# Kernel tuning notes

Hardware: AMD Instinct MI355X
Metric: run time of the kernel (lower is better)

The kernel has to match this reference:

```python
import jax, jax.numpy as jnp
import numpy as np

N_NODES = 50000
N_EDGES = 800000
HEADS = 2
HID = 64
NEG_SLOPE = 0.2


def setup_inputs() -> dict:
    key = jax.random.key(0)
    ks = jax.random.split(key, 8)
    x = jax.random.normal(ks[0], (N_NODES, 128), dtype=jnp.float32)
    W_src = jax.random.normal(ks[1], (128, HEADS * HID), dtype=jnp.float32) * (1.0 / np.sqrt(128))
    W_dst = jax.random.normal(ks[2], (128, HEADS * HID), dtype=jnp.float32) * (1.0 / np.sqrt(128))
    att_src = jax.random.normal(ks[3], (HEADS, HID), dtype=jnp.float32) * 0.1
    att_dst = jax.random.normal(ks[4], (HEADS, HID), dtype=jnp.float32) * 0.1
    bias = jax.random.normal(ks[5], (HEADS * HID,), dtype=jnp.float32) * 0.01
    prelu_w = jnp.full((HEADS * HID,), 0.25, dtype=jnp.float32)
    edge_index = jax.random.randint(ks[6], (2, N_EDGES), 0, N_NODES, dtype=jnp.int64)
    return {"x": x, "W_src": W_src, "W_dst": W_dst, "att_src": att_src,
            "att_dst": att_dst, "bias": bias, "prelu_w": prelu_w,
            "edge_index": edge_index}


def gat_prelu(x, W_src, W_dst, att_src, att_dst, bias, prelu_w, edge_index):
    N = x.shape[0]
    src, dst = edge_index[0], edge_index[1]
    xs = (x @ W_src).reshape(N, HEADS, HID)   # [N,H,C]
    xd = (x @ W_dst).reshape(N, HEADS, HID)
    a_src = jnp.einsum('nhc,hc->nh', xs, att_src)  # [N,H]
    a_dst = jnp.einsum('nhc,hc->nh', xd, att_dst)
    e = jax.nn.leaky_relu(a_src[src] + a_dst[dst], NEG_SLOPE)  # [E,H]
    # segment softmax over incoming edges of each dst node
    m = jax.ops.segment_max(e, dst, num_segments=N)            # [N,H]
    ee = jnp.exp(e - m[dst])
    denom = jax.ops.segment_sum(ee, dst, num_segments=N)
    alpha = ee / (denom[dst] + 1e-16)                          # [E,H]
    msg = xs[src] * alpha[:, :, None]                          # [E,H,C]
    out = jax.ops.segment_sum(msg, dst, num_segments=N)        # [N,H,C]
    out = out.reshape(N, HEADS * HID) + bias
    return jnp.where(out >= 0, out, prelu_w * out)


def reference(x, W_src, W_dst, att_src, att_dst, bias, prelu_w, edge_index):
    return gat_prelu(x, W_src, W_dst, att_src, att_dst, bias, prelu_w, edge_index)
```

## Files before the change

### kernel.cpp

```cpp
#include <hip/hip_runtime.h>
#include <hip/hip_fp16.h>


#define N_NODES 50000
#define N_EDGES 800000
#define CAP     56
#define BSH     8
#define NB      196
#define CHUNK   4096
#define NBLK    196
#define CCAP    64

#define OFF_A      0
#define OFF_CNT    800000
#define OFF_XS     1000256
#define OFF_BKT    13800256
#define OFF_SWZ    36200256
#define DOUT_COARSE 0
#define DOUT_CELL   19668992

typedef _Float16 f16x8 __attribute__((ext_vector_type(8)));
typedef float    f32x4 __attribute__((ext_vector_type(4)));
typedef unsigned long long u64;

__global__ __launch_bounds__(256) void k0_prep(
    const float* __restrict__ Wsrc, const float* __restrict__ Wdst,
    const float* __restrict__ att_s, const float* __restrict__ att_d,
    __half* __restrict__ swz)
{
    __shared__ float vS[128 * 4];
    const int nt = blockIdx.x;
    const int t = threadIdx.x;
    if (nt == 8) {
        if (t < 128) {
            const float* wsp = Wsrc + t * 128;
            const float* wdp = Wdst + t * 128;
            float a0 = 0.f, a1 = 0.f, a2 = 0.f, a3 = 0.f;
#pragma unroll 8
            for (int c = 0; c < 64; ++c) {
                a0 += wsp[c]      * att_s[c];
                a1 += wsp[64 + c] * att_s[64 + c];
                a2 += wdp[c]      * att_d[c];
                a3 += wdp[64 + c] * att_d[64 + c];
            }
            *(float4*)(vS + t * 4) = make_float4(a0, a1, a2, a3);
        }
        __syncthreads();
    }
    const int kb = t >> 6, L = t & 63;
    const int col = L & 15;
    const int krow = kb * 32 + ((L >> 4) & 3) * 8;
    f16x8 v;
    if (nt < 8) {
#pragma unroll
        for (int j = 0; j < 8; ++j)
            v[j] = (_Float16)Wsrc[(size_t)(krow + j) * 128 + nt * 16 + col];
    } else {
#pragma unroll
        for (int j = 0; j < 8; ++j)
            v[j] = (col < 4) ? (_Float16)vS[(krow + j) * 4 + col] : (_Float16)0.f;
    }
    *(f16x8*)(swz + ((size_t)(kb * 9 + nt) * 64 + L) * 8) = v;
}

__global__ __launch_bounds__(256) void k1_gemm(
    const float* __restrict__ x, const __half* __restrict__ swz,
    __half* __restrict__ xs, float* __restrict__ a_all)
{
    __shared__ __half tile[64 * 136];
    const int t = threadIdx.x;
    const int w = t >> 6, L = t & 63;
    const int m = L & 15, q = L >> 4;
    const int n_a = blockIdx.x * 64 + w * 16 + m;
    const int rrow = (n_a < N_NODES) ? n_a : (N_NODES - 1);
    const float* xrow = x + (size_t)rrow * 128;

    f32x4 acc[9];
#pragma unroll
    for (int nt = 0; nt < 9; ++nt) acc[nt] = (f32x4){0.f, 0.f, 0.f, 0.f};

#pragma unroll
    for (int kb = 0; kb < 4; ++kb) {
        const int k0 = kb * 32 + q * 8;
        float4 xa = *(const float4*)(xrow + k0);
        float4 xb = *(const float4*)(xrow + k0 + 4);
        f16x8 a;
        a[0] = (_Float16)xa.x; a[1] = (_Float16)xa.y;
        a[2] = (_Float16)xa.z; a[3] = (_Float16)xa.w;
        a[4] = (_Float16)xb.x; a[5] = (_Float16)xb.y;
        a[6] = (_Float16)xb.z; a[7] = (_Float16)xb.w;
        const f16x8* bbase = (const f16x8*)swz + (size_t)(kb * 9) * 64 + L;
#pragma unroll
        for (int nt = 0; nt < 9; ++nt) {
            f16x8 b = bbase[(size_t)nt * 64];
            acc[nt] = __builtin_amdgcn_mfma_f32_16x16x32_f16(a, b, acc[nt], 0, 0, 0);
        }
    }

    const int rloc = w * 16 + q * 4;
#pragma unroll
    for (int nt = 0; nt < 8; ++nt) {
#pragma unroll
        for (int r = 0; r < 4; ++r)
            tile[(rloc + r) * 136 + nt * 16 + m] = (__half)acc[nt][r];
    }
    __syncthreads();
    const int n0 = blockIdx.x * 64;
#pragma unroll
    for (int cc = 0; cc < 4; ++cc) {
        int task = cc * 256 + t;
        int row = task >> 4, ch = (task & 15) * 8;
        int n = n0 + row;
        if (n < N_NODES) {
            ulonglong2 v = *(const ulonglong2*)(tile + row * 136 + ch);
            *(ulonglong2*)(xs + (size_t)n * 128 + ch) = v;
        }
    }

    if (m < 4) {
#pragma unroll
        for (int r = 0; r < 4; ++r) {
            int n = n0 + rloc + r;
            if (n < N_NODES) a_all[(size_t)n * 4 + m] = acc[8][r];
        }
    }
}

__global__ __launch_bounds__(256) void kB_bin(
    const int* __restrict__ ei, const float* __restrict__ a_all,
    u64* __restrict__ coarse, int* __restrict__ cellcnt)
{
    __shared__ int lcnt[NB];
    const int t = threadIdx.x;
    if (t < NB) lcnt[t] = 0;
    __syncthreads();
    const int e0 = blockIdx.x * CHUNK;
#pragma unroll
    for (int u = 0; u < 8; ++u) {
        int e = e0 + u * 512 + t * 2;
        if (e < N_EDGES) {
            int2 ss = *(const int2*)(ei + e);
            int2 dd = *(const int2*)(ei + N_EDGES + e);
            float2 as0 = *(const float2*)(a_all + (size_t)ss.x * 4);
            float2 ad0 = *(const float2*)(a_all + (size_t)dd.x * 4 + 2);
            float2 as1 = *(const float2*)(a_all + (size_t)ss.y * 4);
            float2 ad1 = *(const float2*)(a_all + (size_t)dd.y * 4 + 2);
            float e00 = as0.x + ad0.x, e01 = as0.y + ad0.y;
            float e10 = as1.x + ad1.x, e11 = as1.y + ad1.y;
            e00 = (e00 >= 0.f) ? e00 : 0.2f * e00;
            e01 = (e01 >= 0.f) ? e01 : 0.2f * e01;
            e10 = (e10 >= 0.f) ? e10 : 0.2f * e10;
            e11 = (e11 >= 0.f) ? e11 : 0.2f * e11;
            __half2 hw0 = __floats2half2_rn(__expf(e00), __expf(e01));
            __half2 hw1 = __floats2half2_rn(__expf(e10), __expf(e11));
            unsigned lo0 = (unsigned)ss.x | ((unsigned)(dd.x & 255) << 16);
            unsigned lo1 = (unsigned)ss.y | ((unsigned)(dd.y & 255) << 16);
            u64 ent0 = (u64)lo0 | ((u64)*reinterpret_cast<unsigned*>(&hw0) << 32);
            u64 ent1 = (u64)lo1 | ((u64)*reinterpret_cast<unsigned*>(&hw1) << 32);
            int b0 = dd.x >> BSH, b1 = dd.y >> BSH;
            int p0 = atomicAdd(&lcnt[b0], 1);
            int p1 = atomicAdd(&lcnt[b1], 1);
            if (p0 < CCAP)
                coarse[((size_t)b0 * NBLK + blockIdx.x) * CCAP + p0] = ent0;
            if (p1 < CCAP)
                coarse[((size_t)b1 * NBLK + blockIdx.x) * CCAP + p1] = ent1;
        }
    }
    __syncthreads();
    if (t < NB) {
        int c = lcnt[t];
        cellcnt[t * NBLK + blockIdx.x] = (c < CCAP) ? c : CCAP;
    }
}

__global__ __launch_bounds__(512) void kD_fine(
    const u64* __restrict__ coarse, const int* __restrict__ cellcnt,
    int* __restrict__ cnt, int2* __restrict__ bkt)
{
    __shared__ int cur[256];
    __shared__ int ccnt[NBLK];
    const int b = blockIdx.x, t = threadIdx.x;
    if (t < 256) cur[t] = 0;
    if (t < NBLK) ccnt[t] = cellcnt[b * NBLK + t];
    __syncthreads();
    const u64* src = coarse + (size_t)b * NBLK * CCAP;
    const int HALF = CCAP / 2;
    for (int g2 = t; g2 < NBLK * HALF; g2 += 512) {
        int c = g2 >> 5, sp = (g2 & 31) * 2;
        int cc = ccnt[c];
        if (sp < cc) {
            ulonglong2 pr = *(const ulonglong2*)(src + (size_t)c * CCAP + sp);
            {
                unsigned lo = (unsigned)pr.x;
                int drel = (lo >> 16) & 255;
                int pos = atomicAdd(&cur[drel], 1);
                if (pos < CAP) {
                    int d = (b << BSH) + drel;
                    bkt[(size_t)d * CAP + pos] =
                        make_int2((int)(lo & 0xFFFF), (int)(unsigned)(pr.x >> 32));
                }
            }
            if (sp + 1 < cc) {
                unsigned lo = (unsigned)pr.y;
                int drel = (lo >> 16) & 255;
                int pos = atomicAdd(&cur[drel], 1);
                if (pos < CAP) {
                    int d = (b << BSH) + drel;
                    bkt[(size_t)d * CAP + pos] =
                        make_int2((int)(lo & 0xFFFF), (int)(unsigned)(pr.y >> 32));
                }
            }
        }
    }
    __syncthreads();
    if (t < 256) {
        int d = (b << BSH) + t;
        if (d < N_NODES) cnt[d] = cur[t];
    }
}

template<bool GUARD>
__device__ __forceinline__ void pstep4(const int2* __restrict__ row, int k, int m,
                                       int sh, int j, const __half* __restrict__ xs,
                                       float& ax, float& ay, float& sw)
{
    int4 p0 = *(const int4*)(row + k);
    int4 p1 = *(const int4*)(row + k + 2);
    int s0 = p0.x, s1 = p0.z, s2 = p1.x, s3 = p1.z;
    unsigned w0 = (unsigned)p0.y, w1 = (unsigned)p0.w;
    unsigned w2 = (unsigned)p1.y, w3 = (unsigned)p1.w;
    if (GUARD) {
        if (k + 0 >= m) { s0 = 0; w0 = 0; }
        if (k + 1 >= m) { s1 = 0; w1 = 0; }
        if (k + 2 >= m) { s2 = 0; w2 = 0; }
        if (k + 3 >= m) { s3 = 0; w3 = 0; }
    }
    __half2 h0 = *(const __half2*)(xs + (size_t)s0 * 128 + j);
    __half2 h1 = *(const __half2*)(xs + (size_t)s1 * 128 + j);
    __half2 h2 = *(const __half2*)(xs + (size_t)s2 * 128 + j);
    __half2 h3 = *(const __half2*)(xs + (size_t)s3 * 128 + j);
    float a0 = __half2float(__ushort_as_half((unsigned short)(w0 >> sh)));
    float a1 = __half2float(__ushort_as_half((unsigned short)(w1 >> sh)));
    float a2 = __half2float(__ushort_as_half((unsigned short)(w2 >> sh)));
    float a3 = __half2float(__ushort_as_half((unsigned short)(w3 >> sh)));
    ax += __half2float(h0.x) * a0; ay += __half2float(h0.y) * a0;
    ax += __half2float(h1.x) * a1; ay += __half2float(h1.y) * a1;
    ax += __half2float(h2.x) * a2; ay += __half2float(h2.y) * a2;
    ax += __half2float(h3.x) * a3; ay += __half2float(h3.y) * a3;
    sw += (a0 + a1) + (a2 + a3);
}

__global__ __launch_bounds__(256) void k6_pass(
    const int2* __restrict__ bkt, const int* __restrict__ cnt,
    const __half* __restrict__ xs, const float* __restrict__ bias,
    const float* __restrict__ prelu_w, float* __restrict__ out)
{
    const int pass = blockIdx.x & 3;
    const int grp  = blockIdx.x >> 2;
    const int t = threadIdx.x;
    const int w = t >> 6, lane = t & 63;
    const int q = lane >> 4, l16 = lane & 15;
    const int node = grp * 16 + w * 4 + q;
    const int j = pass * 32 + l16 * 2;
    const int sh = (pass & 2) ? 16 : 0;
    int m = 0;
    if (node < N_NODES) { m = cnt[node]; if (m > CAP) m = CAP; }
    const int2* row = bkt + (size_t)node * CAP;
    float ax = 0.f, ay = 0.f, sw = 0.f;
    int k = 0;
    for (; k + 4 <= m; k += 4)
        pstep4<false>(row, k, m, sh, j, xs, ax, ay, sw);
    if (k < m)
        pstep4<true>(row, k, m, sh, j, xs, ax, ay, sw);

    if (node < N_NODES) {
        float inv = 1.f / (sw + 1e-16f);
        float o0 = ax * inv + bias[j];
        float o1 = ay * inv + bias[j + 1];
        float2 r;
        r.x = (o0 >= 0.f) ? o0 : prelu_w[j] * o0;
        r.y = (o1 >= 0.f) ? o1 : prelu_w[j + 1] * o1;
        *(float2*)(out + (size_t)node * 128 + j) = r;
    }
}

extern "C" void kernel_launch(void* const* d_in, const int* in_sizes, int n_in,
                              void* d_out, int out_size, void* d_ws, size_t ws_size,
                              hipStream_t stream) {
    const float* x      = (const float*)d_in[0];
    const float* Wsrc   = (const float*)d_in[1];
    const float* Wdst   = (const float*)d_in[2];
    const float* att_s  = (const float*)d_in[3];
    const float* att_d  = (const float*)d_in[4];
    const float* bias   = (const float*)d_in[5];
    const float* prelu  = (const float*)d_in[6];
    const int*   ei     = (const int*)d_in[7];
    float* out = (float*)d_out;

    char* ws = (char*)d_ws;
    float*  a_all  = (float*)(ws + OFF_A);
    int*    cnt    = (int*)(ws + OFF_CNT);
    __half* xs     = (__half*)(ws + OFF_XS);
    int2*   bkt    = (int2*)(ws + OFF_BKT);
    __half* swz    = (__half*)(ws + OFF_SWZ);

    char* outb = (char*)d_out;
    u64* coarse  = (u64*)(outb + DOUT_COARSE);
    int* cellcnt = (int*)(outb + DOUT_CELL);

    k0_prep<<<9, 256, 0, stream>>>(Wsrc, Wdst, att_s, att_d, swz);
    k1_gemm<<<(N_NODES + 63) / 64, 256, 0, stream>>>(x, swz, xs, a_all);
    kB_bin<<<NBLK, 256, 0, stream>>>(ei, a_all, coarse, cellcnt);
    kD_fine<<<NB, 512, 0, stream>>>(coarse, cellcnt, cnt, bkt);
    k6_pass<<<4 * ((N_NODES + 15) / 16), 256, 0, stream>>>(bkt, cnt, xs, bias, prelu, out);
}
```

Baseline: 181.2 us.

## Split xs into per-pass column planes and gather eight edges per step

The projected feature table xs is stored as four planes of 32 halves per node, one per pass, instead of 128-wide rows. Each k6_pass block then gathers from a compact 64-byte-per-node plane, which should improve cache locality for the random source gathers. The inner loop is also unrolled from 4 to 8 edges per step, putting more loads in flight. The cost is more register pressure and a guarded tail that can waste up to 7 masked loads per node.

```diff
diff --git a/kernel.cpp b/kernel.cpp
--- a/kernel.cpp
+++ b/kernel.cpp
@@ -109,11 +109,11 @@
 #pragma unroll
     for (int cc = 0; cc < 4; ++cc) {
         int task = cc * 256 + t;
-        int row = task >> 4, ch = (task & 15) * 8;
+        int row = task >> 4, ch = task & 15;
         int n = n0 + row;
         if (n < N_NODES) {
-            ulonglong2 v = *(const ulonglong2*)(tile + row * 136 + ch);
-            *(ulonglong2*)(xs + (size_t)n * 128 + ch) = v;
+            ulonglong2 v = *(const ulonglong2*)(tile + row * 136 + ch * 8);
+            *(ulonglong2*)(xs + ((size_t)(ch >> 2) * N_NODES + n) * 32 + (ch & 3) * 8) = v;
         }
     }
 
@@ -220,34 +220,55 @@
 }
 
 template<bool GUARD>
-__device__ __forceinline__ void pstep4(const int2* __restrict__ row, int k, int m,
-                                       int sh, int j, const __half* __restrict__ xs,
+__device__ __forceinline__ void pstep8(const int2* __restrict__ row, int k, int m,
+                                       int sh, int c2, const __half* __restrict__ xsp,
                                        float& ax, float& ay, float& sw)
 {
     int4 p0 = *(const int4*)(row + k);
     int4 p1 = *(const int4*)(row + k + 2);
+    int4 p2 = *(const int4*)(row + k + 4);
+    int4 p3 = *(const int4*)(row + k + 6);
     int s0 = p0.x, s1 = p0.z, s2 = p1.x, s3 = p1.z;
+    int s4 = p2.x, s5 = p2.z, s6 = p3.x, s7 = p3.z;
     unsigned w0 = (unsigned)p0.y, w1 = (unsigned)p0.w;
     unsigned w2 = (unsigned)p1.y, w3 = (unsigned)p1.w;
+    unsigned w4 = (unsigned)p2.y, w5 = (unsigned)p2.w;
+    unsigned w6 = (unsigned)p3.y, w7 = (unsigned)p3.w;
     if (GUARD) {
         if (k + 0 >= m) { s0 = 0; w0 = 0; }
         if (k + 1 >= m) { s1 = 0; w1 = 0; }
         if (k + 2 >= m) { s2 = 0; w2 = 0; }
         if (k + 3 >= m) { s3 = 0; w3 = 0; }
-    }
-    __half2 h0 = *(const __half2*)(xs + (size_t)s0 * 128 + j);
-    __half2 h1 = *(const __half2*)(xs + (size_t)s1 * 128 + j);
-    __half2 h2 = *(const __half2*)(xs + (size_t)s2 * 128 + j);
-    __half2 h3 = *(const __half2*)(xs + (size_t)s3 * 128 + j);
+        if (k + 4 >= m) { s4 = 0; w4 = 0; }
+        if (k + 5 >= m) { s5 = 0; w5 = 0; }
+        if (k + 6 >= m) { s6 = 0; w6 = 0; }
+        if (k + 7 >= m) { s7 = 0; w7 = 0; }
+    }
+    __half2 h0 = *(const __half2*)(xsp + (size_t)s0 * 32 + c2);
+    __half2 h1 = *(const __half2*)(xsp + (size_t)s1 * 32 + c2);
+    __half2 h2 = *(const __half2*)(xsp + (size_t)s2 * 32 + c2);
+    __half2 h3 = *(const __half2*)(xsp + (size_t)s3 * 32 + c2);
+    __half2 h4 = *(const __half2*)(xsp + (size_t)s4 * 32 + c2);
+    __half2 h5 = *(const __half2*)(xsp + (size_t)s5 * 32 + c2);
+    __half2 h6 = *(const __half2*)(xsp + (size_t)s6 * 32 + c2);
+    __half2 h7 = *(const __half2*)(xsp + (size_t)s7 * 32 + c2);
     float a0 = __half2float(__ushort_as_half((unsigned short)(w0 >> sh)));
     float a1 = __half2float(__ushort_as_half((unsigned short)(w1 >> sh)));
     float a2 = __half2float(__ushort_as_half((unsigned short)(w2 >> sh)));
     float a3 = __half2float(__ushort_as_half((unsigned short)(w3 >> sh)));
+    float a4 = __half2float(__ushort_as_half((unsigned short)(w4 >> sh)));
+    float a5 = __half2float(__ushort_as_half((unsigned short)(w5 >> sh)));
+    float a6 = __half2float(__ushort_as_half((unsigned short)(w6 >> sh)));
+    float a7 = __half2float(__ushort_as_half((unsigned short)(w7 >> sh)));
     ax += __half2float(h0.x) * a0; ay += __half2float(h0.y) * a0;
     ax += __half2float(h1.x) * a1; ay += __half2float(h1.y) * a1;
     ax += __half2float(h2.x) * a2; ay += __half2float(h2.y) * a2;
     ax += __half2float(h3.x) * a3; ay += __half2float(h3.y) * a3;
-    sw += (a0 + a1) + (a2 + a3);
+    ax += __half2float(h4.x) * a4; ay += __half2float(h4.y) * a4;
+    ax += __half2float(h5.x) * a5; ay += __half2float(h5.y) * a5;
+    ax += __half2float(h6.x) * a6; ay += __half2float(h6.y) * a6;
+    ax += __half2float(h7.x) * a7; ay += __half2float(h7.y) * a7;
+    sw += ((a0 + a1) + (a2 + a3)) + ((a4 + a5) + (a6 + a7));
 }
 
 __global__ __launch_bounds__(256) void k6_pass(
@@ -261,17 +282,19 @@
     const int w = t >> 6, lane = t & 63;
     const int q = lane >> 4, l16 = lane & 15;
     const int node = grp * 16 + w * 4 + q;
-    const int j = pass * 32 + l16 * 2;
+    const int c2 = l16 * 2;
+    const int j = pass * 32 + c2;
     const int sh = (pass & 2) ? 16 : 0;
+    const __half* xsp = xs + (size_t)pass * N_NODES * 32;
     int m = 0;
     if (node < N_NODES) { m = cnt[node]; if (m > CAP) m = CAP; }
     const int2* row = bkt + (size_t)node * CAP;
     float ax = 0.f, ay = 0.f, sw = 0.f;
     int k = 0;
-    for (; k + 4 <= m; k += 4)
-        pstep4<false>(row, k, m, sh, j, xs, ax, ay, sw);
+    for (; k + 8 <= m; k += 8)
+        pstep8<false>(row, k, m, sh, c2, xsp, ax, ay, sw);
     if (k < m)
-        pstep4<true>(row, k, m, sh, j, xs, ax, ay, sw);
+        pstep8<true>(row, k, m, sh, c2, xsp, ax, ay, sw);
 
     if (node < N_NODES) {
         float inv = 1.f / (sw + 1e-16f);
```

Result: faster. 171.1 us (-5.6%).

## Split xs into per-pass planes and pad buckets for 8-edge prefetched gather

Applied to the files above, without the earlier changes.

The GEMM now writes the fp16 projected features as four planar 32-column slices, one per pass, so each k6 pass gathers from a compact 50000x32 plane instead of strided 128-wide rows. This is meant to improve cache locality for the gather. The fine-binning kernel zero-pads each bucket row up to a multiple of 8 edges, which lets the aggregation loop process 8 edges per iteration with no guard and software-prefetch the next 8 bucket entries. The grid is also sized to exactly N/16 groups, dropping bounds checks, which relies on N being divisible by 16.

```diff
diff --git a/kernel.cpp b/kernel.cpp
--- a/kernel.cpp
+++ b/kernel.cpp
@@ -109,11 +109,11 @@
 #pragma unroll
     for (int cc = 0; cc < 4; ++cc) {
         int task = cc * 256 + t;
-        int row = task >> 4, ch = (task & 15) * 8;
+        int row = task >> 4, ch = task & 15;
         int n = n0 + row;
         if (n < N_NODES) {
-            ulonglong2 v = *(const ulonglong2*)(tile + row * 136 + ch);
-            *(ulonglong2*)(xs + (size_t)n * 128 + ch) = v;
+            ulonglong2 v = *(const ulonglong2*)(tile + row * 136 + ch * 8);
+            *(ulonglong2*)(xs + ((size_t)(ch >> 2) * N_NODES + n) * 32 + (ch & 3) * 8) = v;
         }
     }
 
@@ -215,39 +215,15 @@
     __syncthreads();
     if (t < 256) {
         int d = (b << BSH) + t;
-        if (d < N_NODES) cnt[d] = cur[t];
-    }
-}
-
-template<bool GUARD>
-__device__ __forceinline__ void pstep4(const int2* __restrict__ row, int k, int m,
-                                       int sh, int j, const __half* __restrict__ xs,
-                                       float& ax, float& ay, float& sw)
-{
-    int4 p0 = *(const int4*)(row + k);
-    int4 p1 = *(const int4*)(row + k + 2);
-    int s0 = p0.x, s1 = p0.z, s2 = p1.x, s3 = p1.z;
-    unsigned w0 = (unsigned)p0.y, w1 = (unsigned)p0.w;
-    unsigned w2 = (unsigned)p1.y, w3 = (unsigned)p1.w;
-    if (GUARD) {
-        if (k + 0 >= m) { s0 = 0; w0 = 0; }
-        if (k + 1 >= m) { s1 = 0; w1 = 0; }
-        if (k + 2 >= m) { s2 = 0; w2 = 0; }
-        if (k + 3 >= m) { s3 = 0; w3 = 0; }
-    }
-    __half2 h0 = *(const __half2*)(xs + (size_t)s0 * 128 + j);
-    __half2 h1 = *(const __half2*)(xs + (size_t)s1 * 128 + j);
-    __half2 h2 = *(const __half2*)(xs + (size_t)s2 * 128 + j);
-    __half2 h3 = *(const __half2*)(xs + (size_t)s3 * 128 + j);
-    float a0 = __half2float(__ushort_as_half((unsigned short)(w0 >> sh)));
-    float a1 = __half2float(__ushort_as_half((unsigned short)(w1 >> sh)));
-    float a2 = __half2float(__ushort_as_half((unsigned short)(w2 >> sh)));
-    float a3 = __half2float(__ushort_as_half((unsigned short)(w3 >> sh)));
-    ax += __half2float(h0.x) * a0; ay += __half2float(h0.y) * a0;
-    ax += __half2float(h1.x) * a1; ay += __half2float(h1.y) * a1;
-    ax += __half2float(h2.x) * a2; ay += __half2float(h2.y) * a2;
-    ax += __half2float(h3.x) * a3; ay += __half2float(h3.y) * a3;
-    sw += (a0 + a1) + (a2 + a3);
+        if (d < N_NODES) {
+            int c = cur[t];
+            cnt[d] = c;
+            int cc = (c < CAP) ? c : CAP;
+            int ce = (cc + 7) & ~7;
+            int2* r = bkt + (size_t)d * CAP;
+            for (int p = cc; p < ce; ++p) r[p] = make_int2(0, 0);
+        }
+    }
 }
 
 __global__ __launch_bounds__(256) void k6_pass(
@@ -261,27 +237,64 @@
     const int w = t >> 6, lane = t & 63;
     const int q = lane >> 4, l16 = lane & 15;
     const int node = grp * 16 + w * 4 + q;
-    const int j = pass * 32 + l16 * 2;
+    const int c2 = l16 * 2;
+    const int j = pass * 32 + c2;
     const int sh = (pass & 2) ? 16 : 0;
-    int m = 0;
-    if (node < N_NODES) { m = cnt[node]; if (m > CAP) m = CAP; }
-    const int2* row = bkt + (size_t)node * CAP;
+    const __half* xsp = xs + pass * (N_NODES * 32);
+
+    int m = cnt[node]; if (m > CAP) m = CAP;
+    const int mr = (m + 7) & ~7;
+    const int4* row = (const int4*)(bkt + node * CAP);
+
     float ax = 0.f, ay = 0.f, sw = 0.f;
-    int k = 0;
-    for (; k + 4 <= m; k += 4)
-        pstep4<false>(row, k, m, sh, j, xs, ax, ay, sw);
-    if (k < m)
-        pstep4<true>(row, k, m, sh, j, xs, ax, ay, sw);
-
-    if (node < N_NODES) {
-        float inv = 1.f / (sw + 1e-16f);
-        float o0 = ax * inv + bias[j];
-        float o1 = ay * inv + bias[j + 1];
-        float2 r;
-        r.x = (o0 >= 0.f) ? o0 : prelu_w[j] * o0;
-        r.y = (o1 >= 0.f) ? o1 : prelu_w[j + 1] * o1;
-        *(float2*)(out + (size_t)node * 128 + j) = r;
-    }
+    if (mr) {
+        int4 e0 = row[0], e1 = row[1], e2 = row[2], e3 = row[3];
+        int k = 0;
+        for (;;) {
+            const bool more = (k + 8 < mr);
+            int4 f0, f1, f2, f3;
+            if (more) {
+                const int4* nrow = row + ((k + 8) >> 1);
+                f0 = nrow[0]; f1 = nrow[1]; f2 = nrow[2]; f3 = nrow[3];
+            }
+            __half2 h0 = *(const __half2*)(xsp + e0.x * 32 + c2);
+            __half2 h1 = *(const __half2*)(xsp + e0.z * 32 + c2);
+            __half2 h2 = *(const __half2*)(xsp + e1.x * 32 + c2);
+            __half2 h3 = *(const __half2*)(xsp + e1.z * 32 + c2);
+            __half2 h4 = *(const __half2*)(xsp + e2.x * 32 + c2);
+            __half2 h5 = *(const __half2*)(xsp + e2.z * 32 + c2);
+            __half2 h6 = *(const __half2*)(xsp + e3.x * 32 + c2);
+            __half2 h7 = *(const __half2*)(xsp + e3.z * 32 + c2);
+            float a0 = __half2float(__ushort_as_half((unsigned short)(((unsigned)e0.y) >> sh)));
+            float a1 = __half2float(__ushort_as_half((unsigned short)(((unsigned)e0.w) >> sh)));
+            float a2 = __half2float(__ushort_as_half((unsigned short)(((unsigned)e1.y) >> sh)));
+            float a3 = __half2float(__ushort_as_half((unsigned short)(((unsigned)e1.w) >> sh)));
+            float a4 = __half2float(__ushort_as_half((unsigned short)(((unsigned)e2.y) >> sh)));
+            float a5 = __half2float(__ushort_as_half((unsigned short)(((unsigned)e2.w) >> sh)));
+            float a6 = __half2float(__ushort_as_half((unsigned short)(((unsigned)e3.y) >> sh)));
+            float a7 = __half2float(__ushort_as_half((unsigned short)(((unsigned)e3.w) >> sh)));
+            ax += __half2float(h0.x) * a0; ay += __half2float(h0.y) * a0;
+            ax += __half2float(h1.x) * a1; ay += __half2float(h1.y) * a1;
+            ax += __half2float(h2.x) * a2; ay += __half2float(h2.y) * a2;
+            ax += __half2float(h3.x) * a3; ay += __half2float(h3.y) * a3;
+            ax += __half2float(h4.x) * a4; ay += __half2float(h4.y) * a4;
+            ax += __half2float(h5.x) * a5; ay += __half2float(h5.y) * a5;
+            ax += __half2float(h6.x) * a6; ay += __half2float(h6.y) * a6;
+            ax += __half2float(h7.x) * a7; ay += __half2float(h7.y) * a7;
+            sw += ((a0 + a1) + (a2 + a3)) + ((a4 + a5) + (a6 + a7));
+            k += 8;
+            if (k >= mr) break;
+            e0 = f0; e1 = f1; e2 = f2; e3 = f3;
+        }
+    }
+
+    float inv = 1.f / (sw + 1e-16f);
+    float o0 = ax * inv + bias[j];
+    float o1 = ay * inv + bias[j + 1];
+    float2 r;
+    r.x = (o0 >= 0.f) ? o0 : prelu_w[j] * o0;
+    r.y = (o1 >= 0.f) ? o1 : prelu_w[j + 1] * o1;
+    *(float2*)(out + (size_t)node * 128 + j) = r;
 }
 
 extern "C" void kernel_launch(void* const* d_in, const int* in_sizes, int n_in,
@@ -312,5 +325,5 @@
     k1_gemm<<<(N_NODES + 63) / 64, 256, 0, stream>>>(x, swz, xs, a_all);
     kB_bin<<<NBLK, 256, 0, stream>>>(ei, a_all, coarse, cellcnt);
     kD_fine<<<NB, 512, 0, stream>>>(coarse, cellcnt, cnt, bkt);
-    k6_pass<<<4 * ((N_NODES + 15) / 16), 256, 0, stream>>>(bkt, cnt, xs, bias, prelu, out);
-}
+    k6_pass<<<4 * (N_NODES / 16), 256, 0, stream>>>(bkt, cnt, xs, bias, prelu, out);
+}
```

Measured after the change: 168.9 us. 1.07x faster.
